# Performance work log

Hardware: AMD Instinct MI355X
Metric: run time of the kernel (lower is better)

## Reference

```python
import jax, jax.numpy as jnp
import numpy as np

N, VW, DW, VP, DP, H, M = 1024, 50000, 300, 50, 100, 512, 256


def _run_dir(x, Wih, Whh, b, reverse):
    # Single-direction LSTM over [n, in] -> [n, H]. PyTorch gate order i,f,g,o.
    Hh = Whh.shape[1]
    def step(carry, xt):
        h, c = carry
        z = xt @ Wih.T + h @ Whh.T + b  # [4H]
        i, f, g, o = jnp.split(z, 4, axis=-1)
        c = jax.nn.sigmoid(f) * c + jax.nn.sigmoid(i) * jnp.tanh(g)
        h = jax.nn.sigmoid(o) * jnp.tanh(c)
        return (h, c), h
    init = (jnp.zeros((Hh,), x.dtype), jnp.zeros((Hh,), x.dtype))
    _, hs = jax.lax.scan(step, init, x, reverse=reverse)
    return hs


def setup_inputs() -> dict:
    key = jax.random.key(0)
    ks = jax.random.split(key, 24)
    s = 0.05  # small init to keep tanh/sigmoid unsaturated
    d = {
        "word_idx": jax.random.randint(ks[0], (N,), 0, VW, dtype=jnp.int32),
        "pos_idx": jax.random.randint(ks[1], (N,), 0, VP, dtype=jnp.int32),
        "word_emb": jax.random.normal(ks[2], (VW, DW), jnp.float32) * s,
        "pos_emb": jax.random.normal(ks[3], (VP, DP), jnp.float32) * s,
        "wih0f": jax.random.normal(ks[4], (4 * H, DW + DP), jnp.float32) * s,
        "whh0f": jax.random.normal(ks[5], (4 * H, H), jnp.float32) * s,
        "b0f": jax.random.normal(ks[6], (4 * H,), jnp.float32) * s,
        "wih0r": jax.random.normal(ks[7], (4 * H, DW + DP), jnp.float32) * s,
        "whh0r": jax.random.normal(ks[8], (4 * H, H), jnp.float32) * s,
        "b0r": jax.random.normal(ks[9], (4 * H,), jnp.float32) * s,
        "wih1f": jax.random.normal(ks[10], (4 * H, 2 * H), jnp.float32) * s,
        "whh1f": jax.random.normal(ks[11], (4 * H, H), jnp.float32) * s,
        "b1f": jax.random.normal(ks[12], (4 * H,), jnp.float32) * s,
        "wih1r": jax.random.normal(ks[13], (4 * H, 2 * H), jnp.float32) * s,
        "whh1r": jax.random.normal(ks[14], (4 * H, H), jnp.float32) * s,
        "b1r": jax.random.normal(ks[15], (4 * H,), jnp.float32) * s,
        "W1": jax.random.normal(ks[16], (M, 4 * H), jnp.float32) * s,
        "bmlp1": jax.random.normal(ks[17], (M,), jnp.float32) * s,
        "w2": jax.random.normal(ks[18], (1, M), jnp.float32) * s,
        "b2": jax.random.normal(ks[19], (1,), jnp.float32) * s,
    }
    return d


def reference(word_idx, pos_idx, word_emb, pos_emb,
              wih0f, whh0f, b0f, wih0r, whh0r, b0r,
              wih1f, whh1f, b1f, wih1r, whh1r, b1r,
              W1, bmlp1, w2, b2):
    # Embed words + pos, concat -> [n, 400]
    x = jnp.concatenate([word_emb[word_idx], pos_emb[pos_idx]], axis=1)
    # 2-layer bidirectional LSTM encoder (batch of 1 squeezed away, as in the module)
    h0 = jnp.concatenate([_run_dir(x, wih0f, whh0f, b0f, False),
                          _run_dir(x, wih0r, whh0r, b0r, True)], axis=1)   # [n, 2H]
    h1 = jnp.concatenate([_run_dir(h0, wih1f, whh1f, b1f, False),
                          _run_dir(h0, wih1r, whh1r, b1r, True)], axis=1)  # [n, 2H]
    # Pairwise MLP score: MLP(concat(h_i, h_j)). Split W1 into head/dep halves so the
    # big GEMM is done once per token instead of once per pair (same math).
    twoH = h1.shape[1]
    a = h1 @ W1[:, :twoH].T            # [n, M], contribution of h_i
    bpart = h1 @ W1[:, twoH:].T        # [n, M], contribution of h_j
    hidden = jnp.tanh(a[:, None, :] + bpart[None, :, :] + bmlp1)  # [n, n, M]
    scores = hidden @ w2[0] + b2[0]    # [n, n]
    return scores
```

## Files before the change

### kernel.cpp

```cpp
#include <hip/hip_runtime.h>
#include <hip/hip_bf16.h>

#define HID   512
#define SEQ   1024
#define WGD   32
#define GATES 2048

__device__ __forceinline__ float sigm(float x) {
    return 1.f / (1.f + __expf(-x));
}
__device__ __forceinline__ float tanh_fast(float x) {
    float ax = fabsf(x);
    float e  = __expf(-2.f * ax);
    float t  = (1.f - e) * __builtin_amdgcn_rcpf(1.f + e);
    return copysignf(t, x);
}
__device__ __forceinline__ float bcast(float v, int l) {
    return __uint_as_float((unsigned)__builtin_amdgcn_readlane((int)__float_as_uint(v), l));
}

__global__ void embed_kernel(const int* __restrict__ wi, const int* __restrict__ pi,
                             const float* __restrict__ we, const float* __restrict__ pe,
                             float* __restrict__ x) {
    int i = blockIdx.x;
    int t = threadIdx.x;
    const float* w = we + (size_t)wi[i] * 300;
    const float* p = pe + (size_t)pi[i] * 100;
    float* xo = x + (size_t)i * 400;
    for (int c = t; c < 300; c += 128) xo[c]       = w[c];
    for (int c = t; c < 100; c += 128) xo[300 + c] = p[c];
}

__global__ __launch_bounds__(256)
void gemm_bias(const float* __restrict__ A, const float* __restrict__ B,
               const float* __restrict__ bias, float* __restrict__ C,
               int M, int N, int K, int lda, int ldb, int ldc) {
    __shared__ float As[64 * 17];
    __shared__ float Bs[64 * 17];
    const int tid  = threadIdx.x;
    const int bn   = blockIdx.x, bm = blockIdx.y;
    const int tj   = tid & 15, ti = tid >> 4;
    const int lrow = tid >> 2;
    const int lk4  = (tid & 3) << 2;
    float acc[4][4] = {};

    for (int kt = 0; kt < K; kt += 16) {
        float4 av = *(const float4*)(A + (size_t)(bm * 64 + lrow) * lda + kt + lk4);
        float4 bv = *(const float4*)(B + (size_t)(bn * 64 + lrow) * ldb + kt + lk4);
        As[lrow * 17 + lk4 + 0] = av.x; As[lrow * 17 + lk4 + 1] = av.y;
        As[lrow * 17 + lk4 + 2] = av.z; As[lrow * 17 + lk4 + 3] = av.w;
        Bs[lrow * 17 + lk4 + 0] = bv.x; Bs[lrow * 17 + lk4 + 1] = bv.y;
        Bs[lrow * 17 + lk4 + 2] = bv.z; Bs[lrow * 17 + lk4 + 3] = bv.w;
        __syncthreads();
        #pragma unroll
        for (int k = 0; k < 16; ++k) {
            float a0 = As[(ti * 4 + 0) * 17 + k];
            float a1 = As[(ti * 4 + 1) * 17 + k];
            float a2 = As[(ti * 4 + 2) * 17 + k];
            float a3 = As[(ti * 4 + 3) * 17 + k];
            float b0 = Bs[(tj * 4 + 0) * 17 + k];
            float b1 = Bs[(tj * 4 + 1) * 17 + k];
            float b2_ = Bs[(tj * 4 + 2) * 17 + k];
            float b3 = Bs[(tj * 4 + 3) * 17 + k];
            acc[0][0] = fmaf(a0, b0, acc[0][0]); acc[0][1] = fmaf(a0, b1, acc[0][1]);
            acc[0][2] = fmaf(a0, b2_, acc[0][2]); acc[0][3] = fmaf(a0, b3, acc[0][3]);
            acc[1][0] = fmaf(a1, b0, acc[1][0]); acc[1][1] = fmaf(a1, b1, acc[1][1]);
            acc[1][2] = fmaf(a1, b2_, acc[1][2]); acc[1][3] = fmaf(a1, b3, acc[1][3]);
            acc[2][0] = fmaf(a2, b0, acc[2][0]); acc[2][1] = fmaf(a2, b1, acc[2][1]);
            acc[2][2] = fmaf(a2, b2_, acc[2][2]); acc[2][3] = fmaf(a2, b3, acc[2][3]);
            acc[3][0] = fmaf(a3, b0, acc[3][0]); acc[3][1] = fmaf(a3, b1, acc[3][1]);
            acc[3][2] = fmaf(a3, b2_, acc[3][2]); acc[3][3] = fmaf(a3, b3, acc[3][3]);
        }
        __syncthreads();
    }
    const int n0 = bn * 64 + tj * 4;
    float bb0 = 0.f, bb1 = 0.f, bb2 = 0.f, bb3 = 0.f;
    if (bias) { bb0 = bias[n0]; bb1 = bias[n0 + 1]; bb2 = bias[n0 + 2]; bb3 = bias[n0 + 3]; }
    #pragma unroll
    for (int i = 0; i < 4; ++i) {
        float4 o;
        o.x = acc[i][0] + bb0; o.y = acc[i][1] + bb1;
        o.z = acc[i][2] + bb2; o.w = acc[i][3] + bb3;
        *(float4*)(C + (size_t)(bm * 64 + ti * 4 + i) * ldc + n0) = o;
    }
}

__global__ __launch_bounds__(512)
void lstm_layer(const float* __restrict__ Zf, const float* __restrict__ Zr,
                const float* __restrict__ WhhF, const float* __restrict__ WhhR,
                unsigned long long* __restrict__ Hpair,
                float* __restrict__ Hout,
                unsigned tagBase) {
    const int dir = blockIdx.x >> 5;
    const int wg  = blockIdx.x & 31;
    const float* __restrict__ Z   = dir ? Zr   : Zf;
    const float* __restrict__ Whh = dir ? WhhR : WhhF;
    const int colOff = dir ? HID : 0;

    const int tid  = threadIdx.x;
    const int wave = tid >> 6;
    const int lane = tid & 63;
    const int g    = lane >> 4;
    const int jj   = lane & 15;
    const int grow = g * HID + wg * 16 + jj;

    float w[64];
    {
        const float4* wp = (const float4*)(Whh + (size_t)grow * HID + wave * 64);
        #pragma unroll
        for (int q = 0; q < 16; ++q) {
            float4 v = wp[q];
            w[4 * q] = v.x; w[4 * q + 1] = v.y; w[4 * q + 2] = v.z; w[4 * q + 3] = v.w;
        }
    }

    __shared__ float part[8 * 65];
    float cval = 0.f;

    for (int s = 0; s < SEQ; ++s) {
        const int t = dir ? (SEQ - 1 - s) : s;

        float zin = 0.f;
        if (wave == 0) zin = Z[(size_t)t * GATES + grow];

        float acc = 0.f;
        if (s > 0) {
            const int tp = dir ? (t + 1) : (t - 1);
            const unsigned expTag = tagBase + (unsigned)s - 1u;
            unsigned long long* hp = Hpair + (size_t)tp * (2 * HID) + colOff + wave * 64;
            unsigned long long* op = Hpair + (size_t)tp * (2 * HID) + colOff + wg * 16 + jj;
            unsigned long long v, o;
            for (;;) {
                v = __hip_atomic_load(hp + lane, __ATOMIC_RELAXED, __HIP_MEMORY_SCOPE_AGENT);
                o = __hip_atomic_load(op,        __ATOMIC_RELAXED, __HIP_MEMORY_SCOPE_AGENT);
                int ok = ((unsigned)(v >> 32) == expTag) & ((unsigned)(o >> 32) == expTag);
                if (__all(ok)) break;
            }
            float hv = __uint_as_float((unsigned)v);
            float a0 = 0.f, a1 = 0.f, a2 = 0.f, a3 = 0.f;
            #pragma unroll
            for (int m = 0; m < 64; m += 4) {
                a0 = fmaf(w[m + 0], bcast(hv, m + 0), a0);
                a1 = fmaf(w[m + 1], bcast(hv, m + 1), a1);
                a2 = fmaf(w[m + 2], bcast(hv, m + 2), a2);
                a3 = fmaf(w[m + 3], bcast(hv, m + 3), a3);
            }
            acc = (a0 + a1) + (a2 + a3);
        }
        part[wave * 65 + lane] = acc;
        __syncthreads();

        if (wave == 0) {
            float r = zin;
            #pragma unroll
            for (int c = 0; c < 8; ++c) r += part[c * 65 + lane];
            float zi = __shfl(r, jj);
            float zf = __shfl(r, 16 + jj);
            float zg = __shfl(r, 32 + jj);
            float zo = __shfl(r, 48 + jj);
            if (lane < 16) {
                float ig = sigm(zi), fg = sigm(zf), gg = tanh_fast(zg), og = sigm(zo);
                cval = fg * cval + ig * gg;
                float hv = og * tanh_fast(cval);
                const size_t oidx = (size_t)t * (2 * HID) + colOff + wg * 16 + lane;
                unsigned long long pk = ((unsigned long long)(tagBase + (unsigned)s) << 32)
                                      | (unsigned long long)__float_as_uint(hv);
                __hip_atomic_store(Hpair + oidx, pk, __ATOMIC_RELAXED, __HIP_MEMORY_SCOPE_AGENT);
                Hout[oidx] = hv;
            }
        }
    }
}

__global__ __launch_bounds__(256)
void pairwise_kernel(const float* __restrict__ Ah, const float* __restrict__ Bd,
                     const float* __restrict__ w2, const float* __restrict__ b2,
                     float* __restrict__ out) {
    __shared__ __align__(16) float at[16 * 260];
    __shared__ __align__(16) float bt[16 * 260];
    __shared__ __align__(16) float wl[256];
    const int tid = threadIdx.x;
    const int i0 = blockIdx.y * 16, j0 = blockIdx.x * 16;
    for (int u = tid; u < 16 * 256; u += 256) {
        int r = u >> 8, m = u & 255;
        at[r * 260 + m] = Ah[(size_t)(i0 + r) * 256 + m];
        bt[r * 260 + m] = Bd[(size_t)(j0 + r) * 256 + m];
    }
    wl[tid] = w2[tid];
    __syncthreads();
    const int tj = tid & 15, ti = tid >> 4;
    float acc = b2[0];
    #pragma unroll 2
    for (int m = 0; m < 256; m += 4) {
        float4 a4 = *(const float4*)&at[ti * 260 + m];
        float4 b4 = *(const float4*)&bt[tj * 260 + m];
        float4 w4 = *(const float4*)&wl[m];
        acc += tanh_fast(a4.x + b4.x) * w4.x;
        acc += tanh_fast(a4.y + b4.y) * w4.y;
        acc += tanh_fast(a4.z + b4.z) * w4.z;
        acc += tanh_fast(a4.w + b4.w) * w4.w;
    }
    out[(size_t)(i0 + ti) * 1024 + (j0 + tj)] = acc;
}

extern "C" void kernel_launch(void* const* d_in, const int* in_sizes, int n_in,
                              void* d_out, int out_size, void* d_ws, size_t ws_size,
                              hipStream_t stream) {
    const int*   wi    = (const int*)  d_in[0];
    const int*   pi    = (const int*)  d_in[1];
    const float* we    = (const float*)d_in[2];
    const float* pe    = (const float*)d_in[3];
    const float* wih0f = (const float*)d_in[4];
    const float* whh0f = (const float*)d_in[5];
    const float* b0f   = (const float*)d_in[6];
    const float* wih0r = (const float*)d_in[7];
    const float* whh0r = (const float*)d_in[8];
    const float* b0r   = (const float*)d_in[9];
    const float* wih1f = (const float*)d_in[10];
    const float* whh1f = (const float*)d_in[11];
    const float* b1f   = (const float*)d_in[12];
    const float* wih1r = (const float*)d_in[13];
    const float* whh1r = (const float*)d_in[14];
    const float* b1r   = (const float*)d_in[15];
    const float* W1    = (const float*)d_in[16];
    const float* bmlp1 = (const float*)d_in[17];
    const float* w2    = (const float*)d_in[18];
    const float* b2    = (const float*)d_in[19];
    float* out = (float*)d_out;

    char* wsb = (char*)d_ws;
    float* x  = (float*)(wsb + 512);
    float* zA = x  + (size_t)1024 * 400;
    float* zB = zA + (size_t)1024 * 2048;
    float* h0 = zB + (size_t)1024 * 2048;
    float* h1 = h0 + (size_t)1024 * 1024;
    float* aH = h1 + (size_t)1024 * 1024;
    float* bD = aH + (size_t)1024 * 256;
    unsigned long long* Hpair = (unsigned long long*)(bD + (size_t)1024 * 256);

    embed_kernel<<<dim3(1024), dim3(128), 0, stream>>>(wi, pi, we, pe, x);

    gemm_bias<<<dim3(32, 16), dim3(256), 0, stream>>>(x, wih0f, b0f, zA, 1024, 2048, 400, 400, 400, 2048);
    gemm_bias<<<dim3(32, 16), dim3(256), 0, stream>>>(x, wih0r, b0r, zB, 1024, 2048, 400, 400, 400, 2048);

    lstm_layer<<<dim3(64), dim3(512), 0, stream>>>(zA, zB, whh0f, whh0r, Hpair, h0, 1u);

    gemm_bias<<<dim3(32, 16), dim3(256), 0, stream>>>(h0, wih1f, b1f, zA, 1024, 2048, 1024, 1024, 1024, 2048);
    gemm_bias<<<dim3(32, 16), dim3(256), 0, stream>>>(h0, wih1r, b1r, zB, 1024, 2048, 1024, 1024, 1024, 2048);

    lstm_layer<<<dim3(64), dim3(512), 0, stream>>>(zA, zB, whh1f, whh1r, Hpair, h1, 8192u);

    gemm_bias<<<dim3(4, 16), dim3(256), 0, stream>>>(h1, W1,        bmlp1,   aH, 1024, 256, 1024, 1024, 2048, 256);
    gemm_bias<<<dim3(4, 16), dim3(256), 0, stream>>>(h1, W1 + 1024, nullptr, bD, 1024, 256, 1024, 1024, 2048, 256);

    pairwise_kernel<<<dim3(64, 64), dim3(256), 0, stream>>>(aH, bD, w2, b2, out);
}
```

Before: 3.752 ms.

## Restructure LSTM recurrence: per-wave unit ownership, LDS-broadcast h, shuffle reductions

Each wave now owns two hidden units across all four gates, keeping an 8x8 slice of Whh in registers with the K dimension spread over lanes. Previously each wave held a 64-wide K chunk for 16 units and partial sums were combined through shared memory and a __syncthreads. Now only wave 0 polls the tagged global h vector and copies it into a double-buffered LDS slab. It then signals the other waves through a workgroup-scope flag, and the gate pre-activations are reduced with xor shuffles. The intent is to remove the per-step block barrier and the cross-wave partial-sum pass. The cost is a six-stage cross-lane reduction over eight values, a spin-wait on an LDS flag, and a runtime-indexed register array that may spill.

```diff
diff --git a/kernel.cpp b/kernel.cpp
--- a/kernel.cpp
+++ b/kernel.cpp
@@ -14,9 +14,6 @@
     float e  = __expf(-2.f * ax);
     float t  = (1.f - e) * __builtin_amdgcn_rcpf(1.f + e);
     return copysignf(t, x);
-}
-__device__ __forceinline__ float bcast(float v, int l) {
-    return __uint_as_float((unsigned)__builtin_amdgcn_readlane((int)__float_as_uint(v), l));
 }
 
 __global__ void embed_kernel(const int* __restrict__ wi, const int* __restrict__ pi,
@@ -100,74 +97,98 @@
     const int tid  = threadIdx.x;
     const int wave = tid >> 6;
     const int lane = tid & 63;
-    const int g    = lane >> 4;
-    const int jj   = lane & 15;
-    const int grow = g * HID + wg * 16 + jj;
-
-    float w[64];
-    {
-        const float4* wp = (const float4*)(Whh + (size_t)grow * HID + wave * 64);
-        #pragma unroll
-        for (int q = 0; q < 16; ++q) {
-            float4 v = wp[q];
-            w[4 * q] = v.x; w[4 * q + 1] = v.y; w[4 * q + 2] = v.z; w[4 * q + 3] = v.w;
-        }
-    }
-
-    __shared__ float part[8 * 65];
+    const int Ub   = wg * 16 + wave * 2;
+
+    float w[8][8];
+    #pragma unroll
+    for (int j = 0; j < 8; ++j) {
+        const int row = (j & 3) * HID + Ub + (j >> 2);
+        const float* wp = Whh + (size_t)row * HID + lane;
+        #pragma unroll
+        for (int c = 0; c < 8; ++c) w[j][c] = wp[c * 64];
+    }
+
+    __shared__ float hbuf[2][512];
+    __shared__ int   flag;
+    if (tid == 0) flag = 0;
+    __syncthreads();
+
     float cval = 0.f;
 
     for (int s = 0; s < SEQ; ++s) {
         const int t = dir ? (SEQ - 1 - s) : s;
 
-        float zin = 0.f;
-        if (wave == 0) zin = Z[(size_t)t * GATES + grow];
-
-        float acc = 0.f;
+        float z0 = 0.f, z1 = 0.f, z2 = 0.f, z3 = 0.f;
+        if (lane < 2) {
+            const float* zp = Z + (size_t)t * GATES + Ub + lane;
+            z0 = zp[0]; z1 = zp[512]; z2 = zp[1024]; z3 = zp[1536];
+        }
+
+        float h[8];
         if (s > 0) {
-            const int tp = dir ? (t + 1) : (t - 1);
-            const unsigned expTag = tagBase + (unsigned)s - 1u;
-            unsigned long long* hp = Hpair + (size_t)tp * (2 * HID) + colOff + wave * 64;
-            unsigned long long* op = Hpair + (size_t)tp * (2 * HID) + colOff + wg * 16 + jj;
-            unsigned long long v, o;
-            for (;;) {
-                v = __hip_atomic_load(hp + lane, __ATOMIC_RELAXED, __HIP_MEMORY_SCOPE_AGENT);
-                o = __hip_atomic_load(op,        __ATOMIC_RELAXED, __HIP_MEMORY_SCOPE_AGENT);
-                int ok = ((unsigned)(v >> 32) == expTag) & ((unsigned)(o >> 32) == expTag);
-                if (__all(ok)) break;
+            float* slab = hbuf[s & 1];
+            if (wave == 0) {
+                const int tp = dir ? (t + 1) : (t - 1);
+                const unsigned expTag = tagBase + (unsigned)s - 1u;
+                const unsigned long long* hp = Hpair + (size_t)tp * (2 * HID) + colOff;
+                unsigned long long v[8];
+                for (;;) {
+                    #pragma unroll
+                    for (int c = 0; c < 8; ++c)
+                        v[c] = __hip_atomic_load(hp + c * 64 + lane, __ATOMIC_RELAXED, __HIP_MEMORY_SCOPE_AGENT);
+                    int ok = 1;
+                    #pragma unroll
+                    for (int c = 0; c < 8; ++c) ok &= ((unsigned)(v[c] >> 32) == expTag);
+                    if (__all(ok)) break;
+                }
+                #pragma unroll
+                for (int c = 0; c < 8; ++c) {
+                    h[c] = __uint_as_float((unsigned)v[c]);
+                    slab[c * 64 + lane] = h[c];
+                }
+                __hip_atomic_store(&flag, s, __ATOMIC_RELEASE, __HIP_MEMORY_SCOPE_WORKGROUP);
+            } else {
+                while (__hip_atomic_load(&flag, __ATOMIC_ACQUIRE, __HIP_MEMORY_SCOPE_WORKGROUP) < s) {}
+                #pragma unroll
+                for (int c = 0; c < 8; ++c) h[c] = slab[c * 64 + lane];
             }
-            float hv = __uint_as_float((unsigned)v);
-            float a0 = 0.f, a1 = 0.f, a2 = 0.f, a3 = 0.f;
+        } else {
             #pragma unroll
-            for (int m = 0; m < 64; m += 4) {
-                a0 = fmaf(w[m + 0], bcast(hv, m + 0), a0);
-                a1 = fmaf(w[m + 1], bcast(hv, m + 1), a1);
-                a2 = fmaf(w[m + 2], bcast(hv, m + 2), a2);
-                a3 = fmaf(w[m + 3], bcast(hv, m + 3), a3);
-            }
-            acc = (a0 + a1) + (a2 + a3);
-        }
-        part[wave * 65 + lane] = acc;
-        __syncthreads();
-
-        if (wave == 0) {
-            float r = zin;
+            for (int c = 0; c < 8; ++c) h[c] = 0.f;
+        }
+
+        float d[8];
+        #pragma unroll
+        for (int j = 0; j < 8; ++j) {
+            float a = w[j][0] * h[0];
+            a = fmaf(w[j][1], h[1], a);
+            a = fmaf(w[j][2], h[2], a);
+            a = fmaf(w[j][3], h[3], a);
+            a = fmaf(w[j][4], h[4], a);
+            a = fmaf(w[j][5], h[5], a);
+            a = fmaf(w[j][6], h[6], a);
+            a = fmaf(w[j][7], h[7], a);
+            d[j] = a;
+        }
+        #pragma unroll
+        for (int off = 32; off > 0; off >>= 1) {
             #pragma unroll
-            for (int c = 0; c < 8; ++c) r += part[c * 65 + lane];
-            float zi = __shfl(r, jj);
-            float zf = __shfl(r, 16 + jj);
-            float zg = __shfl(r, 32 + jj);
-            float zo = __shfl(r, 48 + jj);
-            if (lane < 16) {
-                float ig = sigm(zi), fg = sigm(zf), gg = tanh_fast(zg), og = sigm(zo);
-                cval = fg * cval + ig * gg;
-                float hv = og * tanh_fast(cval);
-                const size_t oidx = (size_t)t * (2 * HID) + colOff + wg * 16 + lane;
-                unsigned long long pk = ((unsigned long long)(tagBase + (unsigned)s) << 32)
-                                      | (unsigned long long)__float_as_uint(hv);
-                __hip_atomic_store(Hpair + oidx, pk, __ATOMIC_RELAXED, __HIP_MEMORY_SCOPE_AGENT);
-                Hout[oidx] = hv;
-            }
+            for (int j = 0; j < 8; ++j) d[j] += __shfl_xor(d[j], off, 64);
+        }
+
+        if (lane < 2) {
+            float zi = z0 + d[lane * 4 + 0];
+            float zf = z1 + d[lane * 4 + 1];
+            float zg = z2 + d[lane * 4 + 2];
+            float zo = z3 + d[lane * 4 + 3];
+            float ig = sigm(zi), fg = sigm(zf), gg = tanh_fast(zg), og = sigm(zo);
+            cval = fg * cval + ig * gg;
+            float hv = og * tanh_fast(cval);
+            const size_t oidx = (size_t)t * (2 * HID) + colOff + Ub + lane;
+            unsigned long long pk = ((unsigned long long)(tagBase + (unsigned)s) << 32)
+                                  | (unsigned long long)__float_as_uint(hv);
+            __hip_atomic_store(Hpair + oidx, pk, __ATOMIC_RELAXED, __HIP_MEMORY_SCOPE_AGENT);
+            Hout[oidx] = hv;
         }
     }
 }
```

Result: slower. 6.704 ms (+78.7%).

## Double-buffer LSTM partial sums, drop extra poll load, transpose GEMM smem tiles

Applied to the files above, without the earlier changes.

The LSTM recurrence now alternates between two shared-memory partial-sum buffers by step parity. This removes the hazard that made the extra own-column poll necessary, so each step's spin-wait reads only the one h-vector load instead of two. The GEMM stores its shared tiles k-major with a padded stride so each inner iteration reads one float4 per operand instead of eight scalar LDS reads. The risk is correctness: dropping the second poll relies on the double buffer plus the tag check to keep wave 0's reduction ordered against the next step's writes.

```diff
diff --git a/kernel.cpp b/kernel.cpp
--- a/kernel.cpp
+++ b/kernel.cpp
@@ -3,7 +3,6 @@
 
 #define HID   512
 #define SEQ   1024
-#define WGD   32
 #define GATES 2048
 
 __device__ __forceinline__ float sigm(float x) {
@@ -35,8 +34,8 @@
 void gemm_bias(const float* __restrict__ A, const float* __restrict__ B,
                const float* __restrict__ bias, float* __restrict__ C,
                int M, int N, int K, int lda, int ldb, int ldc) {
-    __shared__ float As[64 * 17];
-    __shared__ float Bs[64 * 17];
+    __shared__ __align__(16) float As[16 * 68];
+    __shared__ __align__(16) float Bs[16 * 68];
     const int tid  = threadIdx.x;
     const int bn   = blockIdx.x, bm = blockIdx.y;
     const int tj   = tid & 15, ti = tid >> 4;
@@ -47,29 +46,23 @@
     for (int kt = 0; kt < K; kt += 16) {
         float4 av = *(const float4*)(A + (size_t)(bm * 64 + lrow) * lda + kt + lk4);
         float4 bv = *(const float4*)(B + (size_t)(bn * 64 + lrow) * ldb + kt + lk4);
-        As[lrow * 17 + lk4 + 0] = av.x; As[lrow * 17 + lk4 + 1] = av.y;
-        As[lrow * 17 + lk4 + 2] = av.z; As[lrow * 17 + lk4 + 3] = av.w;
-        Bs[lrow * 17 + lk4 + 0] = bv.x; Bs[lrow * 17 + lk4 + 1] = bv.y;
-        Bs[lrow * 17 + lk4 + 2] = bv.z; Bs[lrow * 17 + lk4 + 3] = bv.w;
+        As[(lk4 + 0) * 68 + lrow] = av.x; As[(lk4 + 1) * 68 + lrow] = av.y;
+        As[(lk4 + 2) * 68 + lrow] = av.z; As[(lk4 + 3) * 68 + lrow] = av.w;
+        Bs[(lk4 + 0) * 68 + lrow] = bv.x; Bs[(lk4 + 1) * 68 + lrow] = bv.y;
+        Bs[(lk4 + 2) * 68 + lrow] = bv.z; Bs[(lk4 + 3) * 68 + lrow] = bv.w;
         __syncthreads();
         #pragma unroll
         for (int k = 0; k < 16; ++k) {
-            float a0 = As[(ti * 4 + 0) * 17 + k];
-            float a1 = As[(ti * 4 + 1) * 17 + k];
-            float a2 = As[(ti * 4 + 2) * 17 + k];
-            float a3 = As[(ti * 4 + 3) * 17 + k];
-            float b0 = Bs[(tj * 4 + 0) * 17 + k];
-            float b1 = Bs[(tj * 4 + 1) * 17 + k];
-            float b2_ = Bs[(tj * 4 + 2) * 17 + k];
-            float b3 = Bs[(tj * 4 + 3) * 17 + k];
-            acc[0][0] = fmaf(a0, b0, acc[0][0]); acc[0][1] = fmaf(a0, b1, acc[0][1]);
-            acc[0][2] = fmaf(a0, b2_, acc[0][2]); acc[0][3] = fmaf(a0, b3, acc[0][3]);
-            acc[1][0] = fmaf(a1, b0, acc[1][0]); acc[1][1] = fmaf(a1, b1, acc[1][1]);
-            acc[1][2] = fmaf(a1, b2_, acc[1][2]); acc[1][3] = fmaf(a1, b3, acc[1][3]);
-            acc[2][0] = fmaf(a2, b0, acc[2][0]); acc[2][1] = fmaf(a2, b1, acc[2][1]);
-            acc[2][2] = fmaf(a2, b2_, acc[2][2]); acc[2][3] = fmaf(a2, b3, acc[2][3]);
-            acc[3][0] = fmaf(a3, b0, acc[3][0]); acc[3][1] = fmaf(a3, b1, acc[3][1]);
-            acc[3][2] = fmaf(a3, b2_, acc[3][2]); acc[3][3] = fmaf(a3, b3, acc[3][3]);
+            float4 a4 = *(const float4*)&As[k * 68 + ti * 4];
+            float4 b4 = *(const float4*)&Bs[k * 68 + tj * 4];
+            acc[0][0] = fmaf(a4.x, b4.x, acc[0][0]); acc[0][1] = fmaf(a4.x, b4.y, acc[0][1]);
+            acc[0][2] = fmaf(a4.x, b4.z, acc[0][2]); acc[0][3] = fmaf(a4.x, b4.w, acc[0][3]);
+            acc[1][0] = fmaf(a4.y, b4.x, acc[1][0]); acc[1][1] = fmaf(a4.y, b4.y, acc[1][1]);
+            acc[1][2] = fmaf(a4.y, b4.z, acc[1][2]); acc[1][3] = fmaf(a4.y, b4.w, acc[1][3]);
+            acc[2][0] = fmaf(a4.z, b4.x, acc[2][0]); acc[2][1] = fmaf(a4.z, b4.y, acc[2][1]);
+            acc[2][2] = fmaf(a4.z, b4.z, acc[2][2]); acc[2][3] = fmaf(a4.z, b4.w, acc[2][3]);
+            acc[3][0] = fmaf(a4.w, b4.x, acc[3][0]); acc[3][1] = fmaf(a4.w, b4.y, acc[3][1]);
+            acc[3][2] = fmaf(a4.w, b4.z, acc[3][2]); acc[3][3] = fmaf(a4.w, b4.w, acc[3][3]);
         }
         __syncthreads();
     }
@@ -114,7 +107,7 @@
         }
     }
 
-    __shared__ float part[8 * 65];
+    __shared__ float part[2][8 * 65];
     float cval = 0.f;
 
     for (int s = 0; s < SEQ; ++s) {
@@ -127,14 +120,11 @@
         if (s > 0) {
             const int tp = dir ? (t + 1) : (t - 1);
             const unsigned expTag = tagBase + (unsigned)s - 1u;
-            unsigned long long* hp = Hpair + (size_t)tp * (2 * HID) + colOff + wave * 64;
-            unsigned long long* op = Hpair + (size_t)tp * (2 * HID) + colOff + wg * 16 + jj;
-            unsigned long long v, o;
+            const unsigned long long* hp = Hpair + (size_t)tp * (2 * HID) + colOff + wave * 64;
+            unsigned long long v;
             for (;;) {
                 v = __hip_atomic_load(hp + lane, __ATOMIC_RELAXED, __HIP_MEMORY_SCOPE_AGENT);
-                o = __hip_atomic_load(op,        __ATOMIC_RELAXED, __HIP_MEMORY_SCOPE_AGENT);
-                int ok = ((unsigned)(v >> 32) == expTag) & ((unsigned)(o >> 32) == expTag);
-                if (__all(ok)) break;
+                if (__all((unsigned)(v >> 32) == expTag)) break;
             }
             float hv = __uint_as_float((unsigned)v);
             float a0 = 0.f, a1 = 0.f, a2 = 0.f, a3 = 0.f;
@@ -147,13 +137,14 @@
             }
             acc = (a0 + a1) + (a2 + a3);
         }
-        part[wave * 65 + lane] = acc;
+        part[s & 1][wave * 65 + lane] = acc;
         __syncthreads();
 
         if (wave == 0) {
+            const float* pp = part[s & 1];
             float r = zin;
             #pragma unroll
-            for (int c = 0; c < 8; ++c) r += part[c * 65 + lane];
+            for (int c = 0; c < 8; ++c) r += pp[c * 65 + lane];
             float zi = __shfl(r, jj);
             float zf = __shfl(r, 16 + jj);
             float zg = __shfl(r, 32 + jj);
```

Result: faster. 3.492 ms (-6.9%).
